# Kernel optimization log

Measured on AMD Instinct MI355X. Metric: run time of the kernel, lower is better.

Reference implementation:

```python
import jax, jax.numpy as jnp
import numpy as np

LOG_DT_MIN = float(np.log(0.001))
LOG_DT_MAX = float(np.log(0.1))


def setup_inputs() -> dict:
    key = jax.random.key(0)
    k1, k2, k3, k4 = jax.random.split(key, 4)
    H, n = 1024, 32  # n = state_dim // 2
    log_dt = jax.random.uniform(k1, (H,), dtype=jnp.float32) * (LOG_DT_MAX - LOG_DT_MIN) + LOG_DT_MIN
    C_re = jax.random.normal(k2, (H, n), dtype=jnp.float32)
    C_im = jax.random.normal(k3, (H, n), dtype=jnp.float32)
    log_A_re = jax.random.normal(k4, (H, n), dtype=jnp.float32)
    A_im = jnp.ones((H, n), dtype=jnp.float32)
    return {"log_dt": log_dt, "C_re": C_re, "C_im": C_im,
            "log_A_re": log_A_re, "A_im": A_im, "L": 4096}


def reference(log_dt, C_re, C_im, log_A_re, A_im, L):
    dt = jnp.exp(log_dt)                       # (H,)
    C = C_re + 1j * C_im                       # (H, n) complex64
    A = -jnp.exp(log_A_re) + 1j * A_im         # (H, n) complex64
    dtA = A * dt[:, None]                      # (H, n)
    # Vandermonde: exp(dtA) ** l for l in [0, L)
    K = dtA[:, :, None] * jnp.arange(L, dtype=jnp.float32)  # (H, n, L)
    C = C * (jnp.exp(dtA) - 1.0) / A           # (H, n)
    return 2.0 * jnp.einsum('hn,hnl->hl', C, jnp.exp(K)).real  # (H, L)
```

## Files before the change

### kernel.cpp

```cpp
#include <hip/hip_runtime.h>
#include <math.h>

#define BLOCK 256
#define CHUNK 16

__global__ __launch_bounds__(BLOCK) void s4_vandermonde(
    const float* __restrict__ log_dt,
    const float* __restrict__ C_re,
    const float* __restrict__ C_im,
    const float* __restrict__ log_A_re,
    const float* __restrict__ A_im,
    float* __restrict__ out,
    int n, int L)
{
    const int h   = blockIdx.x;
    const int base = blockIdx.y * (BLOCK * CHUNK);
    const int tid = threadIdx.x;

    extern __shared__ float smem[];
    float* s_x  = smem;
    float* s_y  = s_x  + n;
    float* s_cr = s_y  + n;
    float* s_ci = s_cr + n;
    float* s_wr = s_ci + n;
    float* s_wi = s_wr + n;

    for (int i = tid; i < n; i += BLOCK) {
        const float dt  = __expf(log_dt[h]);
        const float Are = -__expf(log_A_re[(size_t)h * n + i]);
        const float Aim = A_im[(size_t)h * n + i];
        const float x = Are * dt;
        const float y = Aim * dt;

        float ex = __expf(x), sy, cy;
        __sincosf(y, &sy, &cy);
        const float er = ex * cy, ei = ex * sy;

        const float numr = er - 1.0f, numi = ei;
        const float inv  = 1.0f / (Are * Are + Aim * Aim);
        const float dr = (numr * Are + numi * Aim) * inv;
        const float di = (numi * Are - numr * Aim) * inv;
        const float Cr = C_re[(size_t)h * n + i];
        const float Ci = C_im[(size_t)h * n + i];
        s_cr[i] = Cr * dr - Ci * di;
        s_ci[i] = Cr * di + Ci * dr;
        s_x[i] = x;
        s_y[i] = y;

        float exs = __expf(x * (float)BLOCK), ss, cs;
        __sincosf(y * (float)BLOCK, &ss, &cs);
        s_wr[i] = exs * cs;
        s_wi[i] = exs * ss;
    }
    __syncthreads();

    float acc[CHUNK];
#pragma unroll
    for (int j = 0; j < CHUNK; ++j) acc[j] = 0.0f;

    const float fl = (float)(base + tid);

    for (int i = 0; i < n; ++i) {
        const float x = s_x[i], y = s_y[i];
        float e0 = __expf(x * fl), s0, c0;
        __sincosf(y * fl, &s0, &c0);
        const float cr = s_cr[i], ci = s_ci[i];
        float sr = e0 * (cr * c0 - ci * s0);
        float si = e0 * (cr * s0 + ci * c0);
        const float wr = s_wr[i], wi = s_wi[i];
#pragma unroll
        for (int j = 0; j < CHUNK; ++j) {
            acc[j] += sr;
            const float tr = sr * wr - si * wi;
            const float ti = sr * wi + si * wr;
            sr = tr;
            si = ti;
        }
    }

    float* o = out + (size_t)h * L + base + tid;
#pragma unroll
    for (int j = 0; j < CHUNK; ++j) {
        const int l = base + tid + j * BLOCK;
        if (l < L) o[(size_t)j * BLOCK] = 2.0f * acc[j];
    }
}

extern "C" void kernel_launch(void* const* d_in, const int* in_sizes, int n_in,
                              void* d_out, int out_size, void* d_ws, size_t ws_size,
                              hipStream_t stream) {
    const float* log_dt   = (const float*)d_in[0];
    const float* C_re     = (const float*)d_in[1];
    const float* C_im     = (const float*)d_in[2];
    const float* log_A_re = (const float*)d_in[3];
    const float* A_im     = (const float*)d_in[4];
    float* out = (float*)d_out;

    const int H = in_sizes[0];
    const int n = in_sizes[1] / H;
    const int L = out_size / H;

    const int lchunks = (L + BLOCK * CHUNK - 1) / (BLOCK * CHUNK);
    dim3 grid(H, lchunks);
    const size_t lds = (size_t)6 * n * sizeof(float);
    s4_vandermonde<<<grid, BLOCK, lds, stream>>>(
        log_dt, C_re, C_im, log_A_re, A_im, out, n, L);
}
```

Baseline: 98.26 us.

## Use Chebyshev-style real recurrence with packed float2 FMA over mode pairs

Replaces the complex multiply recurrence with a second-order real recurrence r_{j+1} = 2Re(W) r_j - |W|^2 r_{j-1}, which needs only the real part and cuts the FLOPs per step. Pairs of modes are processed together in float2 vectors so the compiler can emit packed FMA instructions. Block size is halved and the per-thread chunk doubled, so each thread runs longer recurrences and evaluates the transcendentals fewer times overall. In exchange, the two-term recurrence may accumulate more rounding error over longer chains, and each thread holds more accumulator registers.

```diff
diff --git a/kernel.cpp b/kernel.cpp
--- a/kernel.cpp
+++ b/kernel.cpp
@@ -1,8 +1,10 @@
 #include <hip/hip_runtime.h>
 #include <math.h>
 
-#define BLOCK 256
-#define CHUNK 16
+#define BLOCK 128
+#define CHUNK 32
+
+typedef float f32x2 __attribute__((ext_vector_type(2)));
 
 __global__ __launch_bounds__(BLOCK) void s4_vandermonde(
     const float* __restrict__ log_dt,
@@ -13,9 +15,9 @@
     float* __restrict__ out,
     int n, int L)
 {
-    const int h   = blockIdx.x;
+    const int h    = blockIdx.x;
     const int base = blockIdx.y * (BLOCK * CHUNK);
-    const int tid = threadIdx.x;
+    const int tid  = threadIdx.x;
 
     extern __shared__ float smem[];
     float* s_x  = smem;
@@ -24,6 +26,8 @@
     float* s_ci = s_cr + n;
     float* s_wr = s_ci + n;
     float* s_wi = s_wr + n;
+    float* s_a  = s_wi + n;
+    float* s_nb = s_a  + n;
 
     for (int i = tid; i < n; i += BLOCK) {
         const float dt  = __expf(log_dt[h]);
@@ -49,32 +53,76 @@
 
         float exs = __expf(x * (float)BLOCK), ss, cs;
         __sincosf(y * (float)BLOCK, &ss, &cs);
-        s_wr[i] = exs * cs;
-        s_wi[i] = exs * ss;
+        const float Wr = exs * cs, Wi = exs * ss;
+        s_wr[i] = Wr;
+        s_wi[i] = Wi;
+        s_a[i]  = 2.0f * Wr;
+        s_nb[i] = -(exs * exs);
     }
     __syncthreads();
 
-    float acc[CHUNK];
+    f32x2 acc[CHUNK];
 #pragma unroll
-    for (int j = 0; j < CHUNK; ++j) acc[j] = 0.0f;
+    for (int j = 0; j < CHUNK; ++j) acc[j] = (f32x2)(0.0f);
 
     const float fl = (float)(base + tid);
+    const int npair = n >> 1;
 
-    for (int i = 0; i < n; ++i) {
+    for (int p = 0; p < npair; ++p) {
+        const int i0 = 2 * p, i1 = 2 * p + 1;
+        f32x2 rp, rc;
+        {
+            const float x = s_x[i0], y = s_y[i0];
+            float e0 = __expf(x * fl), s0, c0;
+            __sincosf(y * fl, &s0, &c0);
+            const float cr = s_cr[i0], ci = s_ci[i0];
+            const float sr = e0 * (cr * c0 - ci * s0);
+            const float si = e0 * (cr * s0 + ci * c0);
+            rp.x = sr;
+            rc.x = sr * s_wr[i0] - si * s_wi[i0];
+        }
+        {
+            const float x = s_x[i1], y = s_y[i1];
+            float e0 = __expf(x * fl), s0, c0;
+            __sincosf(y * fl, &s0, &c0);
+            const float cr = s_cr[i1], ci = s_ci[i1];
+            const float sr = e0 * (cr * c0 - ci * s0);
+            const float si = e0 * (cr * s0 + ci * c0);
+            rp.y = sr;
+            rc.y = sr * s_wr[i1] - si * s_wi[i1];
+        }
+        const f32x2 a01  = { s_a[i0],  s_a[i1] };
+        const f32x2 nb01 = { s_nb[i0], s_nb[i1] };
+
+        acc[0] += rp;
+        acc[1] += rc;
+#pragma unroll
+        for (int j = 2; j < CHUNK; ++j) {
+            const f32x2 rn = __builtin_elementwise_fma(a01, rc, nb01 * rp);
+            acc[j] += rn;
+            rp = rc;
+            rc = rn;
+        }
+    }
+    if (n & 1) {
+        const int i = n - 1;
         const float x = s_x[i], y = s_y[i];
         float e0 = __expf(x * fl), s0, c0;
         __sincosf(y * fl, &s0, &c0);
         const float cr = s_cr[i], ci = s_ci[i];
-        float sr = e0 * (cr * c0 - ci * s0);
-        float si = e0 * (cr * s0 + ci * c0);
-        const float wr = s_wr[i], wi = s_wi[i];
+        const float sr = e0 * (cr * c0 - ci * s0);
+        const float si = e0 * (cr * s0 + ci * c0);
+        float rp = sr;
+        float rc = sr * s_wr[i] - si * s_wi[i];
+        const float a = s_a[i], nb = s_nb[i];
+        acc[0].x += rp;
+        acc[1].x += rc;
 #pragma unroll
-        for (int j = 0; j < CHUNK; ++j) {
-            acc[j] += sr;
-            const float tr = sr * wr - si * wi;
-            const float ti = sr * wi + si * wr;
-            sr = tr;
-            si = ti;
+        for (int j = 2; j < CHUNK; ++j) {
+            const float rn = fmaf(a, rc, nb * rp);
+            acc[j].x += rn;
+            rp = rc;
+            rc = rn;
         }
     }
 
@@ -82,7 +130,7 @@
 #pragma unroll
     for (int j = 0; j < CHUNK; ++j) {
         const int l = base + tid + j * BLOCK;
-        if (l < L) o[(size_t)j * BLOCK] = 2.0f * acc[j];
+        if (l < L) o[(size_t)j * BLOCK] = 2.0f * (acc[j].x + acc[j].y);
     }
 }
 
@@ -102,7 +150,7 @@
 
     const int lchunks = (L + BLOCK * CHUNK - 1) / (BLOCK * CHUNK);
     dim3 grid(H, lchunks);
-    const size_t lds = (size_t)6 * n * sizeof(float);
+    const size_t lds = (size_t)8 * n * sizeof(float);
     s4_vandermonde<<<grid, BLOCK, lds, stream>>>(
         log_dt, C_re, C_im, log_A_re, A_im, out, n, L);
 }
```

New measurement: 80.22 us. 1.22x faster.
